# Performance work log

Measured on AMD Instinct MI355X. Metric: run time of the kernel, lower is better.

The kernel has to match this reference:

```python
import jax, jax.numpy as jnp
import numpy as np

B, LQ, E = 4, 8400, 256
HEADS, LEVELS, POINTS = 8, 4, 4
HEAD_DIM = E // HEADS
SHAPES = [(80, 80), (40, 40), (20, 20), (10, 10)]  # (H, W) per level; sum HW = 8400
LV = sum(h * w for h, w in SHAPES)


def setup_inputs() -> dict:
    key = jax.random.key(0)
    ks = jax.random.split(key, 12)
    query = jax.random.normal(ks[0], (B, LQ, E), jnp.float32)
    # per-level normalized reference points in (0.1, 0.9)
    reference_points = 0.1 + 0.8 * jax.random.uniform(ks[1], (B, LQ, LEVELS, 2), jnp.float32)
    value = jax.random.normal(ks[2], (B, LV, E), jnp.float32)
    spatial_shapes = jnp.array(SHAPES, dtype=jnp.int32)
    s = 0.05
    Wv = jax.random.normal(ks[3], (E, E), jnp.float32) * s
    bv = jnp.zeros((E,), jnp.float32)
    Woff = jax.random.normal(ks[4], (E, HEADS * LEVELS * POINTS * 2), jnp.float32) * 0.01
    boff = jax.random.normal(ks[5], (HEADS * LEVELS * POINTS * 2,), jnp.float32) * 0.02
    Wattn = jax.random.normal(ks[6], (E, HEADS * LEVELS * POINTS), jnp.float32) * s
    battn = jnp.zeros((HEADS * LEVELS * POINTS,), jnp.float32)
    Wo = jax.random.normal(ks[7], (E, E), jnp.float32) * s
    bo = jnp.zeros((E,), jnp.float32)
    return dict(query=query, reference_points=reference_points, value=value,
                spatial_shapes=spatial_shapes, Wv=Wv, bv=bv, Woff=Woff, boff=boff,
                Wattn=Wattn, battn=battn, Wo=Wo, bo=bo)


def _bilinear_sample(vflat, x, y, Hl, Wl):
    # vflat: [BH, D, Hl*Wl]; x, y: [BH, N] pixel coords (align_corners=False convention)
    x0f = jnp.floor(x); y0f = jnp.floor(y)
    wx = (x - x0f)[:, None, :]; wy = (y - y0f)[:, None, :]
    x0 = x0f.astype(jnp.int32); y0 = y0f.astype(jnp.int32)

    def gather(ix, iy):
        valid = ((ix >= 0) & (ix < Wl) & (iy >= 0) & (iy < Hl)).astype(vflat.dtype)
        idx = jnp.clip(iy, 0, Hl - 1) * Wl + jnp.clip(ix, 0, Wl - 1)
        g = jnp.take_along_axis(vflat, idx[:, None, :], axis=2)  # [BH, D, N]
        return g * valid[:, None, :]

    v00 = gather(x0, y0); v01 = gather(x0 + 1, y0)
    v10 = gather(x0, y0 + 1); v11 = gather(x0 + 1, y0 + 1)
    return (v00 * (1 - wx) * (1 - wy) + v01 * wx * (1 - wy)
            + v10 * (1 - wx) * wy + v11 * wx * wy)


def _msda_forward(query, reference_points, value, spatial_shapes,
                  Wv, bv, Woff, boff, Wattn, battn, Wo, bo):
    b, lq, _ = query.shape
    v = (value @ Wv + bv).reshape(b, -1, HEADS, HEAD_DIM)
    off = (query @ Woff + boff).reshape(b, lq, HEADS, LEVELS, POINTS, 2)
    aw = (query @ Wattn + battn).reshape(b, lq, HEADS, LEVELS * POINTS)
    aw = jax.nn.softmax(aw, axis=-1).reshape(b, lq, HEADS, LEVELS, POINTS)
    # normalizer (W, H) per level
    norm = jnp.stack([spatial_shapes[:, 1], spatial_shapes[:, 0]], axis=-1).astype(query.dtype)
    # sampling locations in [0,1]: [B, Lq, H, L, P, 2]
    loc = reference_points[:, :, None, :, None, :] + off / norm[None, None, None, :, None, :]

    sampled_levels = []
    start = 0
    for lvl, (Hl, Wl) in enumerate(SHAPES):
        vl = v[:, start:start + Hl * Wl]                      # [B, Hl*Wl, H, D]
        start += Hl * Wl
        vflat = vl.transpose(0, 2, 3, 1).reshape(b * HEADS, HEAD_DIM, Hl * Wl)
        grid = loc[:, :, :, lvl]                              # [B, Lq, H, P, 2]
        grid = grid.transpose(0, 2, 1, 3, 4).reshape(b * HEADS, lq * POINTS, 2)
        g = grid * 2.0 - 1.0                                  # grid_sample convention
        x = (g[..., 0] + 1.0) * (Wl * 0.5) - 0.5
        y = (g[..., 1] + 1.0) * (Hl * 0.5) - 0.5
        s = _bilinear_sample(vflat, x, y, Hl, Wl)             # [BH, D, Lq*P]
        sampled_levels.append(s.reshape(b, HEADS, HEAD_DIM, lq, POINTS))
    sampled = jnp.stack(sampled_levels, axis=-1)              # [B, H, D, Lq, P, L]
    out = jnp.einsum('bhdqpl,bqhlp->bqhd', sampled, aw).reshape(b, lq, E)
    return out @ Wo + bo


def reference(query, reference_points, value, spatial_shapes,
              Wv, bv, Woff, boff, Wattn, battn, Wo, bo):
    return _msda_forward(query, reference_points, value, spatial_shapes,
                         Wv, bv, Woff, boff, Wattn, battn, Wo, bo)
```

## Files before the change

### kernel.cpp

```cpp
#include <hip/hip_runtime.h>
#include <math.h>

#define BB 4
#define LQ 8400
#define NH 8
#define LVTOT 8500
#define HD 32
#define NQB 525

typedef __attribute__((ext_vector_type(8))) short short8;
typedef __attribute__((ext_vector_type(4))) float f32x4;
typedef __attribute__((ext_vector_type(2))) float f32x2;
typedef __attribute__((ext_vector_type(2))) _Float16 half2_t;
typedef __attribute__((ext_vector_type(2))) __fp16 fp16x2_t;
typedef unsigned short ushort_t;

__device__ __forceinline__ ushort_t f2bf(float f) {
    union { float f; unsigned u; } v; v.f = f;
    unsigned r = v.u + 0x7fffu + ((v.u >> 16) & 1u);
    return (ushort_t)(r >> 16);
}
__device__ __forceinline__ float bflo(unsigned u) {
    union { unsigned u; float f; } x; x.u = u << 16; return x.f;
}
__device__ __forceinline__ float bfhi(unsigned u) {
    union { unsigned u; float f; } x; x.u = u & 0xffff0000u; return x.f;
}
__device__ __forceinline__ half2_t ash2(unsigned u) {
    union { unsigned u; half2_t h; } x; x.u = u; return x.h;
}
__device__ __forceinline__ unsigned pk2u(fp16x2_t h) {
    union { fp16x2_t h; unsigned u; } x; x.h = h; return x.u;
}

__device__ __forceinline__ void dma16(const ushort_t* g, ushort_t* l) {
    __builtin_amdgcn_global_load_lds(
        (const __attribute__((address_space(1))) void*)g,
        (__attribute__((address_space(3))) void*)l, 16, 0, 0);
}

__global__ __launch_bounds__(256) void prep_all(
    const float* __restrict__ value, const float* __restrict__ query,
    const float* __restrict__ Wv, const float* __restrict__ Woff,
    const float* __restrict__ Wattn, const float* __restrict__ Wo,
    ushort_t* __restrict__ value_b, ushort_t* __restrict__ query_b,
    ushort_t* __restrict__ BT)
{
    const int bid = blockIdx.x;
    if (bid < 16900) {
        const float* src = (bid < 8500) ? value : query;
        ushort_t* dst = (bid < 8500) ? value_b : query_b;
        int i = (bid < 8500 ? bid : bid - 8500) * 256 + threadIdx.x;
        float4 f = ((const float4*)src)[i];
        ushort4 o;
        o.x = f2bf(f.x); o.y = f2bf(f.y); o.z = f2bf(f.z); o.w = f2bf(f.w);
        ((ushort4*)dst)[i] = o;
    } else {
        int idx = (bid - 16900) * 256 + threadIdx.x;
        int r = idx >> 8, k = idx & 255;
        float v;
        if (r < 256) v = Wv[k * 256 + r];
        else if (r < 640) {
            int n = r - 256;
            v = (n < 256) ? Woff[k * 256 + n] : Wattn[k * 128 + (n - 256)];
        } else v = Wo[k * 256 + (r - 640)];
        BT[idx] = f2bf(v);
    }
}

__device__ __forceinline__ void gemm_core(
    const ushort_t* __restrict__ A, const ushort_t* __restrict__ B, int M,
    int m0, int n0, ushort_t* Asl, ushort_t* Bsl, f32x4 acc[4][4])
{
    const int tid  = threadIdx.x;
    const int wave = tid >> 6, lane = tid & 63;
    const int quad = lane >> 4, mr = lane & 15;
    const int wm   = (wave >> 1) * 64, wn = (wave & 1) * 64;
    const int oct  = lane >> 3;
    const int bseg = lane & 7;

    for (int k0 = 0; k0 < 256; k0 += 64) {
        __syncthreads();
        #pragma unroll
        for (int i = 0; i < 4; i++) {
            int m  = i * 32 + wave * 8 + oct;
            int gs = bseg ^ (m & 7);
            int am = min(m0 + m, M - 1);
            dma16(A + (size_t)am * 256 + k0 + gs * 8,
                  Asl + (size_t)(i * 32 + wave * 8) * 64 + lane * 8);
            int bn = n0 + m;
            dma16(B + (size_t)bn * 256 + k0 + gs * 8,
                  Bsl + (size_t)(i * 32 + wave * 8) * 64 + lane * 8);
        }
        __syncthreads();
        #pragma unroll
        for (int ks = 0; ks < 2; ks++) {
            short8 af[4], bf[4];
            const int ksl = ks * 4 + quad;
            #pragma unroll
            for (int i = 0; i < 4; i++) {
                int m = wm + i * 16 + mr;
                af[i] = *(const short8*)&Asl[m * 64 + (ksl ^ (m & 7)) * 8];
                int n = wn + i * 16 + mr;
                bf[i] = *(const short8*)&Bsl[n * 64 + (ksl ^ (n & 7)) * 8];
            }
            #pragma unroll
            for (int i = 0; i < 4; i++)
                #pragma unroll
                for (int j = 0; j < 4; j++)
                    acc[i][j] = __builtin_amdgcn_mfma_f32_16x16x32_bf16(
                        af[i], bf[j], acc[i][j], 0, 0, 0);
        }
    }
}

__global__ __launch_bounds__(256, 3) void gemm_fused(
    const ushort_t* __restrict__ Av, const ushort_t* __restrict__ Aq,
    const ushort_t* __restrict__ BT,
    const float* __restrict__ bv, const float* __restrict__ boff,
    const float* __restrict__ battn,
    ushort_t* __restrict__ vperm, ushort_t* __restrict__ off_b,
    ushort_t* __restrict__ awl_b)
{
    __shared__ ushort_t Asl[128 * 64];
    __shared__ ushort_t Bsl[128 * 64];

    const int bid = blockIdx.x;
    int mode, m0, n0, M;
    const ushort_t *A, *B;
    if (bid < 532) { mode = 0; m0 = (bid >> 1) * 128; n0 = (bid & 1) * 128;
                     A = Av; B = BT; M = 34000; }
    else { int b2 = bid - 532;
           mode = 1; m0 = (b2 / 3) * 128; n0 = (b2 % 3) * 128;
           A = Aq; B = BT + 65536; M = 33600; }

    f32x4 acc[4][4];
    #pragma unroll
    for (int i = 0; i < 4; i++)
        #pragma unroll
        for (int j = 0; j < 4; j++) acc[i][j] = (f32x4){0.f, 0.f, 0.f, 0.f};

    gemm_core(A, B, M, m0, n0, Asl, Bsl, acc);

    const int tid  = threadIdx.x;
    const int wave = tid >> 6, lane = tid & 63;
    const int quad = lane >> 4, mr = lane & 15;
    const int wm   = (wave >> 1) * 64, wn = (wave & 1) * 64;

    #pragma unroll
    for (int i = 0; i < 4; i++) {
        const int rbase = m0 + wm + i * 16 + quad * 4;
        #pragma unroll
        for (int j = 0; j < 4; j++) {
            const int c = n0 + wn + j * 16 + mr;
            #pragma unroll
            for (int reg = 0; reg < 4; reg++) {
                int row = rbase + reg;
                if (row >= M) continue;
                float val = acc[i][j][reg];
                if (mode == 0) {
                    float o = val + bv[c];
                    int b = row / LVTOT, pix = row - b * LVTOT;
                    int h = c >> 5, d = c & 31;
                    union { _Float16 h16; ushort_t u; } cv;
                    cv.h16 = (_Float16)o;
                    vperm[(((size_t)(b * NH + h)) * LVTOT + pix) * HD + d] = cv.u;
                } else {
                    if (c < 256) off_b[(size_t)row * 256 + c] = f2bf(val + boff[c]);
                    else awl_b[(size_t)row * 128 + (c - 256)] = f2bf(val + battn[c - 256]);
                }
            }
        }
    }
}

__global__ __launch_bounds__(256, 3) void gemm_out(
    const ushort_t* __restrict__ A, const ushort_t* __restrict__ BT,
    const float* __restrict__ bo, float* __restrict__ out)
{
    __shared__ ushort_t Asl[128 * 64];
    __shared__ ushort_t Bsl[128 * 64];

    const int m0 = (blockIdx.x >> 1) * 128;
    const int n0 = (blockIdx.x & 1) * 128;
    const int M = 33600;

    f32x4 acc[4][4];
    #pragma unroll
    for (int i = 0; i < 4; i++)
        #pragma unroll
        for (int j = 0; j < 4; j++) acc[i][j] = (f32x4){0.f, 0.f, 0.f, 0.f};

    gemm_core(A, BT, M, m0, n0, Asl, Bsl, acc);

    const int tid  = threadIdx.x;
    const int wave = tid >> 6, lane = tid & 63;
    const int quad = lane >> 4, mr = lane & 15;
    const int wm   = (wave >> 1) * 64, wn = (wave & 1) * 64;

    #pragma unroll
    for (int i = 0; i < 4; i++) {
        const int rbase = m0 + wm + i * 16 + quad * 4;
        #pragma unroll
        for (int j = 0; j < 4; j++) {
            const int c = n0 + wn + j * 16 + mr;
            #pragma unroll
            for (int reg = 0; reg < 4; reg++) {
                int row = rbase + reg;
                if (row >= M) continue;
                out[(size_t)row * 256 + c] = acc[i][j][reg] + bo[c];
            }
        }
    }
}

__global__ __launch_bounds__(1024) void msda_sample(
    const ushort_t* __restrict__ vperm, const ushort_t* __restrict__ off,
    const ushort_t* __restrict__ awl, const float* __restrict__ refp,
    ushort_t* __restrict__ sampled)
{
    __shared__ ushort_t lds_v[2000 * HD];
    __shared__ uint2    s_w[64 * 17];
    __shared__ ushort4  s_iv[64 * 17];

    const int tid   = threadIdx.x;
    const int bid   = blockIdx.x;
    const int h     = bid & 7;
    const int b     = (bid >> 3) & 3;
    const int chunk = bid >> 5;
    const int q0    = chunk * NQB;
    const size_t bq0 = (size_t)b * LQ + q0;

    const ushort_t* plane = vperm + (size_t)(b * NH + h) * (LVTOT * HD);

    {
        const ushort_t* psrc = plane + 6400 * HD;
        #pragma unroll
        for (int it = 0; it < 8; it++) {
            int i = it * 1024 + tid;
            if (i < 8000) dma16(psrc + i * 8, lds_v + i * 8);
        }
    }

    const int Hs[4]    = {80, 40, 20, 10};
    const int base2[4] = {0, 0, 1600, 8400};

    const int NPASS = (NQB + 63) / 64;

    {
        const int ql = tid >> 4, lp = tid & 15;
        const int l  = lp >> 2;
        const int lq = min(ql, NQB - 1);
        const size_t bq = bq0 + lq;
        const int Wl = Hs[l];

        unsigned od = *(const unsigned*)(off + bq * 256 + h * 32 + lp * 2);
        float ox = bflo(od), oy = bfhi(od);
        float lgt = bflo((unsigned)awl[bq * 128 + h * 16 + lp]);
        float e = __expf(lgt);
        float sum = e;
        sum += __shfl_xor(sum, 1, 16);
        sum += __shfl_xor(sum, 2, 16);
        sum += __shfl_xor(sum, 4, 16);
        sum += __shfl_xor(sum, 8, 16);
        float aw = e * __builtin_amdgcn_rcpf(sum);

        float2 rp = *(const float2*)(refp + bq * 8 + l * 2);
        float x = rp.x * (float)Wl + ox - 0.5f;
        float y = rp.y * (float)Wl + oy - 0.5f;
        float x0f = floorf(x), y0f = floorf(y);
        float wx = x - x0f, wy = y - y0f;
        int x0 = (int)x0f, y0 = (int)y0f;
        bool vx0 = (x0 >= 0) & (x0 < Wl);
        bool vx1 = (x0 + 1 >= 0) & (x0 + 1 < Wl);
        bool vy0 = (y0 >= 0) & (y0 < Wl);
        bool vy1 = (y0 + 1 >= 0) & (y0 + 1 < Wl);
        int cx0 = min(max(x0, 0), Wl - 1);
        int cx1 = min(max(x0 + 1, 0), Wl - 1);
        int cy0 = min(max(y0, 0), Wl - 1);
        int cy1 = min(max(y0 + 1, 0), Wl - 1);
        float w00 = (vx0 && vy0) ? (1.f - wx) * (1.f - wy) * aw : 0.f;
        float w01 = (vx1 && vy0) ? wx * (1.f - wy) * aw : 0.f;
        float w10 = (vx0 && vy1) ? (1.f - wx) * wy * aw : 0.f;
        float w11 = (vx1 && vy1) ? wx * wy * aw : 0.f;
        const int rec = ql * 17 + lp;
        const int bs = base2[l];
        s_w[rec] = make_uint2(pk2u(__builtin_amdgcn_cvt_pkrtz(w00, w01)),
                              pk2u(__builtin_amdgcn_cvt_pkrtz(w10, w11)));
        s_iv[rec] = make_ushort4((ushort_t)(bs + cy0 * Wl + cx0),
                                 (ushort_t)(bs + cy0 * Wl + cx1),
                                 (ushort_t)(bs + cy1 * Wl + cx0),
                                 (ushort_t)(bs + cy1 * Wl + cx1));
    }
    __syncthreads();

    for (int p = 0; ; p++) {
        {
            const int ql  = tid >> 4;
            const int sub = tid & 15;
            const int g   = sub >> 3;
            const int dsh = (sub & 7) * 4;
            const int dby = (sub & 7) * 8;
            const int lq  = p * 64 + ql;

            float a0 = 0.f, a1 = 0.f, a2 = 0.f, a3 = 0.f;

            uint2 gw[4]; ushort4 giv[4];
            uint2 gv0[4], gv1[4], gv2[4], gv3[4];
            #pragma unroll
            for (int pi = 0; pi < 4; pi++) {
                const int pt = g ? (12 + pi) : pi;
                const int rec = ql * 17 + pt;
                gw[pi]  = s_w[rec];
                giv[pi] = s_iv[rec];
                gv0[pi] = *(const uint2*)((const char*)plane + (((unsigned)giv[pi].x << 6) + dby));
                gv1[pi] = *(const uint2*)((const char*)plane + (((unsigned)giv[pi].y << 6) + dby));
                gv2[pi] = *(const uint2*)((const char*)plane + (((unsigned)giv[pi].z << 6) + dby));
                gv3[pi] = *(const uint2*)((const char*)plane + (((unsigned)giv[pi].w << 6) + dby));
            }
            #pragma unroll
            for (int pi = 0; pi < 4; pi++) {
                const int pt = g ? (8 + pi) : (4 + pi);
                const int rec = ql * 17 + pt;
                uint2 w = s_w[rec];
                ushort4 iv = s_iv[rec];
                uint2 v0 = *(const uint2*)&lds_v[(unsigned)iv.x * HD + dsh];
                uint2 v1 = *(const uint2*)&lds_v[(unsigned)iv.y * HD + dsh];
                uint2 v2 = *(const uint2*)&lds_v[(unsigned)iv.z * HD + dsh];
                uint2 v3 = *(const uint2*)&lds_v[(unsigned)iv.w * HD + dsh];
                half2_t w01 = ash2(w.x), w23 = ash2(w.y);
                unsigned p01lo = __builtin_amdgcn_perm(v1.x, v0.x, 0x05040100);
                unsigned p01hi = __builtin_amdgcn_perm(v1.x, v0.x, 0x07060302);
                unsigned p23lo = __builtin_amdgcn_perm(v3.x, v2.x, 0x05040100);
                unsigned p23hi = __builtin_amdgcn_perm(v3.x, v2.x, 0x07060302);
                a0 = __builtin_amdgcn_fdot2(w01, ash2(p01lo), a0, false);
                a0 = __builtin_amdgcn_fdot2(w23, ash2(p23lo), a0, false);
                a1 = __builtin_amdgcn_fdot2(w01, ash2(p01hi), a1, false);
                a1 = __builtin_amdgcn_fdot2(w23, ash2(p23hi), a1, false);
                unsigned q01lo = __builtin_amdgcn_perm(v1.y, v0.y, 0x05040100);
                unsigned q01hi = __builtin_amdgcn_perm(v1.y, v0.y, 0x07060302);
                unsigned q23lo = __builtin_amdgcn_perm(v3.y, v2.y, 0x05040100);
                unsigned q23hi = __builtin_amdgcn_perm(v3.y, v2.y, 0x07060302);
                a2 = __builtin_amdgcn_fdot2(w01, ash2(q01lo), a2, false);
                a2 = __builtin_amdgcn_fdot2(w23, ash2(q23lo), a2, false);
                a3 = __builtin_amdgcn_fdot2(w01, ash2(q01hi), a3, false);
                a3 = __builtin_amdgcn_fdot2(w23, ash2(q23hi), a3, false);
            }
            #pragma unroll
            for (int pi = 0; pi < 4; pi++) {
                half2_t w01 = ash2(gw[pi].x), w23 = ash2(gw[pi].y);
                unsigned p01lo = __builtin_amdgcn_perm(gv1[pi].x, gv0[pi].x, 0x05040100);
                unsigned p01hi = __builtin_amdgcn_perm(gv1[pi].x, gv0[pi].x, 0x07060302);
                unsigned p23lo = __builtin_amdgcn_perm(gv3[pi].x, gv2[pi].x, 0x05040100);
                unsigned p23hi = __builtin_amdgcn_perm(gv3[pi].x, gv2[pi].x, 0x07060302);
                a0 = __builtin_amdgcn_fdot2(w01, ash2(p01lo), a0, false);
                a0 = __builtin_amdgcn_fdot2(w23, ash2(p23lo), a0, false);
                a1 = __builtin_amdgcn_fdot2(w01, ash2(p01hi), a1, false);
                a1 = __builtin_amdgcn_fdot2(w23, ash2(p23hi), a1, false);
                unsigned q01lo = __builtin_amdgcn_perm(gv1[pi].y, gv0[pi].y, 0x05040100);
                unsigned q01hi = __builtin_amdgcn_perm(gv1[pi].y, gv0[pi].y, 0x07060302);
                unsigned q23lo = __builtin_amdgcn_perm(gv3[pi].y, gv2[pi].y, 0x05040100);
                unsigned q23hi = __builtin_amdgcn_perm(gv3[pi].y, gv2[pi].y, 0x07060302);
                a2 = __builtin_amdgcn_fdot2(w01, ash2(q01lo), a2, false);
                a2 = __builtin_amdgcn_fdot2(w23, ash2(q23lo), a2, false);
                a3 = __builtin_amdgcn_fdot2(w01, ash2(q01hi), a3, false);
                a3 = __builtin_amdgcn_fdot2(w23, ash2(q23hi), a3, false);
            }
            a0 += __shfl_xor(a0, 8);
            a1 += __shfl_xor(a1, 8);
            a2 += __shfl_xor(a2, 8);
            a3 += __shfl_xor(a3, 8);
            if (sub < 8 && lq < NQB) {
                const size_t bq = bq0 + lq;
                ushort4 o;
                o.x = f2bf(a0); o.y = f2bf(a1);
                o.z = f2bf(a2); o.w = f2bf(a3);
                *(ushort4*)(sampled + bq * 256 + h * 32 + dsh) = o;
            }
        }
        if (p + 1 >= NPASS) break;
        __syncthreads();

        {
            const int ql = tid >> 4, lp = tid & 15;
            const int l  = lp >> 2;
            const int lq = min((p + 1) * 64 + ql, NQB - 1);
            const size_t bq = bq0 + lq;
            const int Wl = Hs[l];

            unsigned od = *(const unsigned*)(off + bq * 256 + h * 32 + lp * 2);
            float ox = bflo(od), oy = bfhi(od);
            float lgt = bflo((unsigned)awl[bq * 128 + h * 16 + lp]);
            float e = __expf(lgt);
            float sum = e;
            sum += __shfl_xor(sum, 1, 16);
            sum += __shfl_xor(sum, 2, 16);
            sum += __shfl_xor(sum, 4, 16);
            sum += __shfl_xor(sum, 8, 16);
            float aw = e * __builtin_amdgcn_rcpf(sum);

            float2 rp = *(const float2*)(refp + bq * 8 + l * 2);
            float x = rp.x * (float)Wl + ox - 0.5f;
            float y = rp.y * (float)Wl + oy - 0.5f;
            float x0f = floorf(x), y0f = floorf(y);
            float wx = x - x0f, wy = y - y0f;
            int x0 = (int)x0f, y0 = (int)y0f;
            bool vx0 = (x0 >= 0) & (x0 < Wl);
            bool vx1 = (x0 + 1 >= 0) & (x0 + 1 < Wl);
            bool vy0 = (y0 >= 0) & (y0 < Wl);
            bool vy1 = (y0 + 1 >= 0) & (y0 + 1 < Wl);
            int cx0 = min(max(x0, 0), Wl - 1);
            int cx1 = min(max(x0 + 1, 0), Wl - 1);
            int cy0 = min(max(y0, 0), Wl - 1);
            int cy1 = min(max(y0 + 1, 0), Wl - 1);
            float w00 = (vx0 && vy0) ? (1.f - wx) * (1.f - wy) * aw : 0.f;
            float w01 = (vx1 && vy0) ? wx * (1.f - wy) * aw : 0.f;
            float w10 = (vx0 && vy1) ? (1.f - wx) * wy * aw : 0.f;
            float w11 = (vx1 && vy1) ? wx * wy * aw : 0.f;
            const int rec = ql * 17 + lp;
            const int bs = base2[l];
            s_w[rec] = make_uint2(pk2u(__builtin_amdgcn_cvt_pkrtz(w00, w01)),
                                  pk2u(__builtin_amdgcn_cvt_pkrtz(w10, w11)));
            s_iv[rec] = make_ushort4((ushort_t)(bs + cy0 * Wl + cx0),
                                     (ushort_t)(bs + cy0 * Wl + cx1),
                                     (ushort_t)(bs + cy1 * Wl + cx0),
                                     (ushort_t)(bs + cy1 * Wl + cx1));
        }
        __syncthreads();
    }
}

extern "C" void kernel_launch(void* const* d_in, const int* in_sizes, int n_in,
                              void* d_out, int out_size, void* d_ws, size_t ws_size,
                              hipStream_t stream) {
    const float* query = (const float*)d_in[0];
    const float* refp  = (const float*)d_in[1];
    const float* value = (const float*)d_in[2];
    const float* Wv    = (const float*)d_in[4];
    const float* bv    = (const float*)d_in[5];
    const float* Woff  = (const float*)d_in[6];
    const float* boff  = (const float*)d_in[7];
    const float* Wattn = (const float*)d_in[8];
    const float* battn = (const float*)d_in[9];
    const float* Wo    = (const float*)d_in[10];
    const float* bo    = (const float*)d_in[11];
    float* out = (float*)d_out;

    ushort_t* ws = (ushort_t*)d_ws;
    ushort_t* off_b   = ws;
    ushort_t* awl_b   = off_b + 8601600;
    ushort_t* value_b = awl_b + 4300800;
    ushort_t* query_b = value_b + 8704000;
    ushort_t* vperm_b = query_b + 8601600;
    ushort_t* BT      = vperm_b + 8704000;
    ushort_t* sampled_b = query_b;

    prep_all<<<dim3(17796), 256, 0, stream>>>(
        value, query, Wv, Woff, Wattn, Wo, value_b, query_b, BT);

    gemm_fused<<<dim3(532 + 789), 256, 0, stream>>>(
        value_b, query_b, BT, bv, boff, battn, vperm_b, off_b, awl_b);

    msda_sample<<<dim3(512), 1024, 0, stream>>>(
        vperm_b, off_b, awl_b, refp, sampled_b);

    gemm_out<<<dim3(526), 256, 0, stream>>>(
        sampled_b, BT + 163840, bo, out);
}
```

Baseline: 248.1 us.

## Double-buffer LDS tiles in GEMM core to overlap global loads with MFMA

The shared GEMM core now stages K-slices into two LDS buffers, issuing the next slice's direct-to-LDS loads before computing on the current one. Explicit vmcnt waits and raw barriers replace the two __syncthreads per iteration. This is meant to hide global load latency behind MFMA work. It doubles LDS per block and lowers the launch-bounds occupancy hint from 3 to 2 blocks, so fewer blocks are resident per CU.

```diff
diff --git a/kernel.cpp b/kernel.cpp
--- a/kernel.cpp
+++ b/kernel.cpp
@@ -79,20 +79,37 @@
     const int oct  = lane >> 3;
     const int bseg = lane & 7;
 
-    for (int k0 = 0; k0 < 256; k0 += 64) {
-        __syncthreads();
+    auto STAGE = [&](int s, int buf) {
+        const int k0 = s * 64;
+        ushort_t* Ad = Asl + buf * (128 * 64);
+        ushort_t* Bd = Bsl + buf * (128 * 64);
         #pragma unroll
         for (int i = 0; i < 4; i++) {
             int m  = i * 32 + wave * 8 + oct;
             int gs = bseg ^ (m & 7);
             int am = min(m0 + m, M - 1);
             dma16(A + (size_t)am * 256 + k0 + gs * 8,
-                  Asl + (size_t)(i * 32 + wave * 8) * 64 + lane * 8);
+                  Ad + (i * 32 + wave * 8) * 64 + lane * 8);
             int bn = n0 + m;
             dma16(B + (size_t)bn * 256 + k0 + gs * 8,
-                  Bsl + (size_t)(i * 32 + wave * 8) * 64 + lane * 8);
-        }
-        __syncthreads();
+                  Bd + (i * 32 + wave * 8) * 64 + lane * 8);
+        }
+    };
+
+    STAGE(0, 0);
+    #pragma unroll
+    for (int t = 0; t < 4; t++) {
+        if (t < 3) {
+            STAGE(t + 1, (t + 1) & 1);
+            asm volatile("s_waitcnt vmcnt(8)" ::: "memory");
+        } else {
+            asm volatile("s_waitcnt vmcnt(0)" ::: "memory");
+        }
+        __builtin_amdgcn_s_barrier();
+        __builtin_amdgcn_sched_barrier(0);
+
+        const ushort_t* As = Asl + (t & 1) * (128 * 64);
+        const ushort_t* Bs = Bsl + (t & 1) * (128 * 64);
         #pragma unroll
         for (int ks = 0; ks < 2; ks++) {
             short8 af[4], bf[4];
@@ -100,9 +117,9 @@
             #pragma unroll
             for (int i = 0; i < 4; i++) {
                 int m = wm + i * 16 + mr;
-                af[i] = *(const short8*)&Asl[m * 64 + (ksl ^ (m & 7)) * 8];
+                af[i] = *(const short8*)&As[m * 64 + (ksl ^ (m & 7)) * 8];
                 int n = wn + i * 16 + mr;
-                bf[i] = *(const short8*)&Bsl[n * 64 + (ksl ^ (n & 7)) * 8];
+                bf[i] = *(const short8*)&Bs[n * 64 + (ksl ^ (n & 7)) * 8];
             }
             #pragma unroll
             for (int i = 0; i < 4; i++)
@@ -111,10 +128,12 @@
                     acc[i][j] = __builtin_amdgcn_mfma_f32_16x16x32_bf16(
                         af[i], bf[j], acc[i][j], 0, 0, 0);
         }
-    }
-}
-
-__global__ __launch_bounds__(256, 3) void gemm_fused(
+        __builtin_amdgcn_sched_barrier(0);
+        __builtin_amdgcn_s_barrier();
+    }
+}
+
+__global__ __launch_bounds__(256, 2) void gemm_fused(
     const ushort_t* __restrict__ Av, const ushort_t* __restrict__ Aq,
     const ushort_t* __restrict__ BT,
     const float* __restrict__ bv, const float* __restrict__ boff,
@@ -122,8 +141,8 @@
     ushort_t* __restrict__ vperm, ushort_t* __restrict__ off_b,
     ushort_t* __restrict__ awl_b)
 {
-    __shared__ ushort_t Asl[128 * 64];
-    __shared__ ushort_t Bsl[128 * 64];
+    __shared__ ushort_t Asl[2 * 128 * 64];
+    __shared__ ushort_t Bsl[2 * 128 * 64];
 
     const int bid = blockIdx.x;
     int mode, m0, n0, M;
@@ -174,12 +193,12 @@
     }
 }
 
-__global__ __launch_bounds__(256, 3) void gemm_out(
+__global__ __launch_bounds__(256, 2) void gemm_out(
     const ushort_t* __restrict__ A, const ushort_t* __restrict__ BT,
     const float* __restrict__ bo, float* __restrict__ out)
 {
-    __shared__ ushort_t Asl[128 * 64];
-    __shared__ ushort_t Bsl[128 * 64];
+    __shared__ ushort_t Asl[2 * 128 * 64];
+    __shared__ ushort_t Bsl[2 * 128 * 64];
 
     const int m0 = (blockIdx.x >> 1) * 128;
     const int n0 = (blockIdx.x & 1) * 128;
```

Result: slower. 269.5 us (+8.6%).
